# Kernel optimization log

Measured on AMD Instinct MI355X. Metric: run time of the kernel, lower is better.

## Reference

```python
import jax, jax.numpy as jnp
import numpy as np

N_HEAD = 16


def setup_inputs() -> dict:
    key = jax.random.key(0)
    k1, k2, k3 = jax.random.split(key, 3)
    B, S, D = 4, 2048, 1024
    scale = 1.0 / np.sqrt(D)
    return {
        "inp": jax.random.normal(k1, (B, S, D), dtype=jnp.float32),
        "w_attn": jax.random.normal(k2, (D, 3 * D), dtype=jnp.float32) * scale,
        "b_attn": jnp.zeros((3 * D,), dtype=jnp.float32),
        "w_proj": jax.random.normal(k3, (D, D), dtype=jnp.float32) * scale,
        "b_proj": jnp.zeros((D,), dtype=jnp.float32),
    }


def reference(inp, w_attn, b_attn, w_proj, b_proj):
    B, S, D = inp.shape
    H = N_HEAD
    hd = D // H
    qkv = inp @ w_attn + b_attn                      # [B,S,3D]
    q, k, v = jnp.split(qkv, 3, axis=-1)
    q = q.reshape(B, S, H, hd)
    k = k.reshape(B, S, H, hd)
    v = v.reshape(B, S, H, hd)
    # scores [B,H,S,S], scaled by 1/sqrt(head_dim)
    scores = jnp.einsum("bqhd,bkhd->bhqk", q, k) / jnp.sqrt(jnp.asarray(hd, dtype=inp.dtype))
    # causal mask: position q attends to k <= q
    causal = jnp.tril(jnp.ones((S, S), dtype=bool))
    scores = jnp.where(causal[None, None], scores, jnp.asarray(-jnp.inf, dtype=scores.dtype))
    probs = jax.nn.softmax(scores, axis=-1)          # dropout omitted (eval mode)
    ctx = jnp.einsum("bhqk,bkhd->bqhd", probs, v).reshape(B, S, D)
    return ctx @ w_proj + b_proj
```

## Files before the change

### kernel.cpp

```cpp
#include <hip/hip_runtime.h>


#define DEV __device__ __forceinline__

typedef unsigned short u16;
typedef unsigned u32x4 __attribute__((ext_vector_type(4)));
typedef u16   u16x8 __attribute__((ext_vector_type(8)));
typedef u16   u16x4 __attribute__((ext_vector_type(4)));
typedef float f32x4v __attribute__((ext_vector_type(4)));
typedef __bf16 bf16x8 __attribute__((ext_vector_type(8)));

#define BB 4
#define SS 2048
#define DD 1024
#define HH 16
#define HD 64
#define MM (BB*SS)
#define N3D (3*DD)
#define C8  0.18033688011112042f

DEV u16 f2bf(float f) { return __builtin_bit_cast(u16, (__bf16)f); }
DEV float bf2f(u16 h) { return __builtin_bit_cast(float, (unsigned)h << 16); }

DEV f32x4v mfma16(u16x8 a, u16x8 b, f32x4v c) {
  return __builtin_amdgcn_mfma_f32_16x16x32_bf16(
      __builtin_bit_cast(bf16x8, a), __builtin_bit_cast(bf16x8, b), c, 0, 0, 0);
}

DEV void async16(const void* g, void* l) {
  __builtin_amdgcn_global_load_lds(
      (const __attribute__((address_space(1))) void*)g,
      (__attribute__((address_space(3))) void*)l, 16, 0, 0);
}

#define WAIT_VM(N) asm volatile("s_waitcnt vmcnt(" #N ")" ::: "memory")
#define BAR() __builtin_amdgcn_s_barrier()

__global__ __launch_bounds__(256) void prep_kernel(
    const float* __restrict__ inp, const float* __restrict__ w_attn,
    const float* __restrict__ w_proj, u16* __restrict__ Abf,
    u16* __restrict__ WAt, u16* __restrict__ WPt) {
  const int bid = blockIdx.x;
  const int tid = threadIdx.x;
  if (bid < 4096) {
    __shared__ float t[32][33];
    const float* W; u16* Wt; int N, K, n0, k0;
    if (bid < 3072) { W = w_attn; Wt = WAt; N = N3D; K = DD;
                      n0 = (bid % 96) * 32; k0 = (bid / 96) * 32; }
    else            { W = w_proj; Wt = WPt; N = DD;  K = DD;
                      int tb = bid - 3072; n0 = (tb % 32) * 32; k0 = (tb / 32) * 32; }
    int tx = tid & 31, ty = tid >> 5;
    for (int i = ty; i < 32; i += 8)
      t[i][tx] = W[(long long)(k0 + i) * N + n0 + tx];
    __syncthreads();
    for (int i = ty; i < 32; i += 8)
      Wt[(long long)(n0 + i) * K + k0 + tx] = f2bf(t[tx][i]);
  } else {
    const long long n = (long long)MM * DD;
    long long i = (long long)(bid - 4096) * 256 + tid;
    for (long long j = i * 4; j < n; j += 2048LL * 256 * 4) {
      f32x4v v = *(const f32x4v*)(inp + j);
      u16x4 o;
      o.x = f2bf(v.x); o.y = f2bf(v.y); o.z = f2bf(v.z); o.w = f2bf(v.w);
      *(u16x4*)(Abf + j) = o;
    }
  }
}

__global__ __launch_bounds__(256) void gemm_kernel(
    const u16* __restrict__ A, const u16* __restrict__ Bt,
    const float* __restrict__ bias, void* __restrict__ Cout,
    u16* __restrict__ Vt, int Ndim, int Kdim, int mode) {
  __shared__ __align__(16) char smem[65536];

  const int tid = threadIdx.x;
  const int lane = tid & 63, wid = tid >> 6;
  const int l15 = lane & 15, lg = lane >> 4;

  const int orig = (int)(blockIdx.y * gridDim.x + blockIdx.x);
  const int xcd = orig & 7;
  const int c = orig >> 3;
  const int st = c >> 6;
  const int byl = (c & 63) >> 3;
  const int bxl = c & 7;
  const int bx = st * 8 + bxl;
  const int by = xcd * 8 + byl;
  const int rb = by * 128, cb = bx * 128;
  const int wr = (wid >> 1) * 64, wc = (wid & 1) * 64;

  f32x4v acc[4][4] = {};

  const int rlo = tid >> 3;
  const int cbS = (tid & 7) * 16;
  const int swS = cbS ^ ((rlo & 7) << 4);
  const int sd  = rlo * 128 + cbS;

  const int xr  = (l15 & 7) << 4;
  const int vaA = l15 * 128 + ((lg * 16) ^ xr);
  const int gvA0 = wr * 128 + vaA, gvA1 = gvA0 ^ 64;
  const int gvB0 = wc * 128 + vaA, gvB1 = gvB0 ^ 64;

  const char* pa[4];
  const char* pb[4];
#pragma unroll
  for (int i = 0; i < 4; ++i) {
    pa[i] = (const char*)A  + (long long)(rb + i * 32 + rlo) * (Kdim * 2) + swS;
    pb[i] = (const char*)Bt + (long long)(cb + i * 32 + rlo) * (Kdim * 2) + swS;
  }

  auto stage = [&](int dofs, int kb) {
#pragma unroll
    for (int i = 0; i < 4; ++i) {
      async16(pa[i] + kb, smem + dofs + i * 4096 + sd);
      async16(pb[i] + kb, smem + 32768 + dofs + i * 4096 + sd);
    }
  };

  auto compute = [&](int aofs, int bofs) {
    u16x8 a0[4], b0[4], a1[4], b1[4];
#pragma unroll
    for (int mi = 0; mi < 4; ++mi) {
      a0[mi] = *(const u16x8*)(smem + aofs + mi * 2048 + gvA0);
      a1[mi] = *(const u16x8*)(smem + aofs + mi * 2048 + gvA1);
    }
#pragma unroll
    for (int ni = 0; ni < 4; ++ni) {
      b0[ni] = *(const u16x8*)(smem + bofs + ni * 2048 + gvB0);
      b1[ni] = *(const u16x8*)(smem + bofs + ni * 2048 + gvB1);
    }
#pragma unroll
    for (int mi = 0; mi < 4; ++mi)
#pragma unroll
      for (int ni = 0; ni < 4; ++ni) {
        acc[mi][ni] = mfma16(a0[mi], b0[ni], acc[mi][ni]);
        acc[mi][ni] = mfma16(a1[mi], b1[ni], acc[mi][ni]);
      }
  };

  const int nK = Kdim >> 6;
  stage(0, 0);
  stage(16384, 128);
  int kt = 0;
  for (; kt + 2 < nK; kt += 2) {
    WAIT_VM(8); BAR();
    compute(0, 32768);
    BAR();
    stage(0, 256);
    WAIT_VM(8); BAR();
    compute(16384, 49152);
    BAR();
    stage(16384, 384);
#pragma unroll
    for (int i = 0; i < 4; ++i) { pa[i] += 256; pb[i] += 256; }
  }
  WAIT_VM(8); BAR();
  compute(0, 32768);
  WAIT_VM(0); BAR();
  compute(16384, 49152);

#pragma unroll
  for (int mi = 0; mi < 4; ++mi)
#pragma unroll
    for (int ni = 0; ni < 4; ++ni) {
      int col = cb + wc + ni * 16 + l15;
      float bv = bias[col];
      if (mode == 1 && col >= 2 * DD) {
        int h = (col >> 6) & 15, d = col & 63;
#pragma unroll
        for (int r = 0; r < 4; ++r) {
          int row = rb + wr + mi * 16 + lg * 4 + r;
          int b = row >> 11, s = row & 2047;
          Vt[(((long long)(b * HH + h) * HD + d) << 11) + s] = f2bf(acc[mi][ni][r] + bv);
        }
      } else {
        float sc = (mode == 1 && col < DD) ? C8 : 1.f;
#pragma unroll
        for (int r = 0; r < 4; ++r) {
          int row = rb + wr + mi * 16 + lg * 4 + r;
          float v = (acc[mi][ni][r] + bv) * sc;
          if (mode) ((u16*)Cout)[(long long)row * Ndim + col] = f2bf(v);
          else      ((float*)Cout)[(long long)row * Ndim + col] = v;
        }
      }
    }
}

__global__ __launch_bounds__(256, 4) void attn_kernel(
    const u16* __restrict__ qkv, const u16* __restrict__ Vt,
    u16* __restrict__ ctx) {
  __shared__ __align__(16) char smem[32768];

  const int tid = threadIdx.x, lane = tid & 63, wid = tid >> 6;
  const int l15 = lane & 15, lg = lane >> 4;

  const int d = (int)blockIdx.x;
  const int rank = d >> 3;
  const int t = rank >> 3;
  const int jj = t & 3, q4 = t >> 2;
  const int qt = (q4 == 0) ? 15 - jj : (q4 == 1) ? 8 + jj
               : (q4 == 2) ? 7 - jj  : jj;
  const int bh = (d & 7) * 8 + (rank & 7);
  const int b = bh >> 4, h = bh & 15;

  const u16* Qcol = qkv + (long long)b * SS * N3D + h * HD;
  const u16* Kcol = qkv + (long long)b * SS * N3D + DD + h * HD;
  const u16* Vbh  = Vt + (long long)bh * HD * SS;

  const u16x8 ones = {0x3F80, 0x3F80, 0x3F80, 0x3F80,
                      0x3F80, 0x3F80, 0x3F80, 0x3F80};

  const int rowA = 8 * (l15 >> 2) + (l15 & 3);
  const int kA = (((l15 & 3) | (((l15 >> 2) & 1) << 2))) << 4;
  const int vk0 = rowA * 128 + ((lg * 16) ^ kA);
  const int vk1 = vk0 ^ 64;
  const int vk2 = vk0 + 512;
  const int vk3 = vk2 ^ 64;
  const int kV = (((l15 & 3) | (((l15 >> 3) & 1) << 2))) << 4;
  const int vv0 = l15 * 128 + ((lg * 16) ^ kV);
  const int vv1 = vv0 ^ 64;

  const int rlo = tid >> 3;
  const int cbS = (tid & 7) * 16;
  const int kw = (((rlo & 3) | (((rlo >> 3) & 1) << 2))) << 4;
  const int swS = cbS ^ kw;
  const int sd  = rlo * 128 + cbS;
  const long long KSTP = 64LL * N3D * 2;
  const long long VSTP = 64LL * 2;
  const long long KHLF = 32LL * N3D * 2;
  const long long VHLF = 32LL * SS * 2;

  auto stage = [&](int dofs, const char* ka, const char* va) {
    async16(ka,        smem + dofs + sd);
    async16(ka + KHLF, smem + dofs + 4096 + sd);
    async16(va,        smem + 16384 + dofs + sd);
    async16(va + VHLF, smem + 16384 + dofs + 4096 + sd);
  };

  const int q0 = qt * 128;
  const int qw = q0 + wid * 32;
  const int nkb = 2 * qt + 2;

  u16x8 qf[2][2];
#pragma unroll
  for (int mi = 0; mi < 2; ++mi)
#pragma unroll
    for (int kk = 0; kk < 2; ++kk)
      qf[mi][kk] = *(const u16x8*)(Qcol + (long long)(qw + mi * 16 + l15) * N3D +
                                   kk * 32 + lg * 8);

  f32x4v acc[2][4] = {};
  f32x4v accl[2] = {};

  const char* ka = (const char*)Kcol + (long long)rlo * (N3D * 2) + swS;
  const char* va = (const char*)Vbh + (long long)rlo * (SS * 2) + swS;

  auto compute = [&](int kofs, int vofs, int kbase) {
    if (kbase > qw + 31) return;

    f32x4v pf[2][2][2] = {};
    {
      u16x8 kf0, kf1;
      kf0 = *(const u16x8*)(smem + kofs + vk0);
      kf1 = *(const u16x8*)(smem + kofs + vk1);
      __builtin_amdgcn_s_setprio(1);
      pf[0][0][0] = mfma16(kf0, qf[0][0], pf[0][0][0]);
      pf[0][0][0] = mfma16(kf1, qf[0][1], pf[0][0][0]);
      pf[1][0][0] = mfma16(kf0, qf[1][0], pf[1][0][0]);
      pf[1][0][0] = mfma16(kf1, qf[1][1], pf[1][0][0]);
      __builtin_amdgcn_s_setprio(0);
      kf0 = *(const u16x8*)(smem + kofs + vk2);
      kf1 = *(const u16x8*)(smem + kofs + vk3);
      __builtin_amdgcn_s_setprio(1);
      pf[0][0][1] = mfma16(kf0, qf[0][0], pf[0][0][1]);
      pf[0][0][1] = mfma16(kf1, qf[0][1], pf[0][0][1]);
      pf[1][0][1] = mfma16(kf0, qf[1][0], pf[1][0][1]);
      pf[1][0][1] = mfma16(kf1, qf[1][1], pf[1][0][1]);
      __builtin_amdgcn_s_setprio(0);
      kf0 = *(const u16x8*)(smem + kofs + 4096 + vk0);
      kf1 = *(const u16x8*)(smem + kofs + 4096 + vk1);
      __builtin_amdgcn_s_setprio(1);
      pf[0][1][0] = mfma16(kf0, qf[0][0], pf[0][1][0]);
      pf[0][1][0] = mfma16(kf1, qf[0][1], pf[0][1][0]);
      pf[1][1][0] = mfma16(kf0, qf[1][0], pf[1][1][0]);
      pf[1][1][0] = mfma16(kf1, qf[1][1], pf[1][1][0]);
      __builtin_amdgcn_s_setprio(0);
      kf0 = *(const u16x8*)(smem + kofs + 4096 + vk2);
      kf1 = *(const u16x8*)(smem + kofs + 4096 + vk3);
      __builtin_amdgcn_s_setprio(1);
      pf[0][1][1] = mfma16(kf0, qf[0][0], pf[0][1][1]);
      pf[0][1][1] = mfma16(kf1, qf[0][1], pf[0][1][1]);
      pf[1][1][1] = mfma16(kf0, qf[1][0], pf[1][1][1]);
      pf[1][1][1] = mfma16(kf1, qf[1][1], pf[1][1][1]);
      __builtin_amdgcn_s_setprio(0);
    }

    if (kbase + 63 > qw) {
      const int kl = kbase + lg * 8;
#pragma unroll
      for (int mi = 0; mi < 2; ++mi) {
        const int qg = qw + mi * 16 + l15;
#pragma unroll
        for (int ks = 0; ks < 2; ++ks)
#pragma unroll
          for (int ab = 0; ab < 2; ++ab)
#pragma unroll
            for (int r = 0; r < 4; ++r)
              if (kl + ks * 32 + ab * 4 + r > qg) pf[mi][ks][ab][r] = -1e30f;
      }
    }

#pragma unroll
    for (int mi = 0; mi < 2; ++mi)
#pragma unroll
      for (int ks = 0; ks < 2; ++ks)
#pragma unroll
        for (int ab = 0; ab < 2; ++ab)
#pragma unroll
          for (int r = 0; r < 4; ++r)
            pf[mi][ks][ab][r] = __builtin_exp2f(pf[mi][ks][ab][r]);

    u16x8 pa[2][2];
#pragma unroll
    for (int mi = 0; mi < 2; ++mi)
#pragma unroll
      for (int ks = 0; ks < 2; ++ks) {
        u32x4 w;
        w.x = (unsigned)f2bf(pf[mi][ks][0][0]) | ((unsigned)f2bf(pf[mi][ks][0][1]) << 16);
        w.y = (unsigned)f2bf(pf[mi][ks][0][2]) | ((unsigned)f2bf(pf[mi][ks][0][3]) << 16);
        w.z = (unsigned)f2bf(pf[mi][ks][1][0]) | ((unsigned)f2bf(pf[mi][ks][1][1]) << 16);
        w.w = (unsigned)f2bf(pf[mi][ks][1][2]) | ((unsigned)f2bf(pf[mi][ks][1][3]) << 16);
        pa[mi][ks] = __builtin_bit_cast(u16x8, w);
      }

    __builtin_amdgcn_s_setprio(1);
    accl[0] = mfma16(pa[0][0], ones, accl[0]);
    accl[0] = mfma16(pa[0][1], ones, accl[0]);
    accl[1] = mfma16(pa[1][0], ones, accl[1]);
    accl[1] = mfma16(pa[1][1], ones, accl[1]);
    __builtin_amdgcn_s_setprio(0);

#pragma unroll
    for (int di = 0; di < 4; ++di) {
      u16x8 v0 = *(const u16x8*)(smem + vofs + di * 2048 + vv0);
      u16x8 v1 = *(const u16x8*)(smem + vofs + di * 2048 + vv1);
      __builtin_amdgcn_s_setprio(1);
      acc[0][di] = mfma16(pa[0][0], v0, acc[0][di]);
      acc[0][di] = mfma16(pa[0][1], v1, acc[0][di]);
      acc[1][di] = mfma16(pa[1][0], v0, acc[1][di]);
      acc[1][di] = mfma16(pa[1][1], v1, acc[1][di]);
      __builtin_amdgcn_s_setprio(0);
    }
  };

  stage(0, ka, va);
  stage(8192, ka + KSTP, va + VSTP);

  int kb = 0;
  for (; kb + 2 < nkb; kb += 2) {
    WAIT_VM(4); BAR();
    compute(0, 16384, kb * 64);
    BAR();
    stage(0, ka + 2 * KSTP, va + 2 * VSTP);
    WAIT_VM(4); BAR();
    compute(8192, 24576, (kb + 1) * 64);
    BAR();
    stage(8192, ka + 3 * KSTP, va + 3 * VSTP);
    ka += 2 * KSTP; va += 2 * VSTP;
  }
  WAIT_VM(4); BAR();
  compute(0, 16384, kb * 64);
  WAIT_VM(0); BAR();
  compute(8192, 24576, (kb + 1) * 64);

#pragma unroll
  for (int mi = 0; mi < 2; ++mi)
#pragma unroll
    for (int r = 0; r < 4; ++r) {
      float inv = 1.f / accl[mi][r];
      int qrow = qw + mi * 16 + lg * 4 + r;
#pragma unroll
      for (int di = 0; di < 4; ++di) {
        int dd = di * 16 + l15;
        ctx[((long long)(b * SS + qrow)) * DD + h * HD + dd] = f2bf(acc[mi][di][r] * inv);
      }
    }
}

extern "C" void kernel_launch(void* const* d_in, const int* in_sizes, int n_in,
                              void* d_out, int out_size, void* d_ws, size_t ws_size,
                              hipStream_t stream) {
  const float* inp    = (const float*)d_in[0];
  const float* w_attn = (const float*)d_in[1];
  const float* b_attn = (const float*)d_in[2];
  const float* w_proj = (const float*)d_in[3];
  const float* b_proj = (const float*)d_in[4];
  float* out = (float*)d_out;
  char* ws = (char*)d_ws;

  const long long off_A   = 0;
  const long long off_WAt = 16777216;
  const long long off_WPt = 23068672;
  const long long off_qkv = 25165824;
  const long long off_ctx = 75497472;
  const long long off_Vt  = 92274688;
  const long long need    = 109051904;
  if (ws_size < (size_t)need) return;

  u16* Abf = (u16*)(ws + off_A);
  u16* WAt = (u16*)(ws + off_WAt);
  u16* WPt = (u16*)(ws + off_WPt);
  u16* qkv = (u16*)(ws + off_qkv);
  u16* ctx = (u16*)(ws + off_ctx);
  u16* Vt  = (u16*)(ws + off_Vt);

  prep_kernel<<<6144, 256, 0, stream>>>(inp, w_attn, w_proj, Abf, WAt, WPt);
  gemm_kernel<<<dim3(N3D / 128, MM / 128), 256, 0, stream>>>(
      Abf, WAt, b_attn, qkv, Vt, N3D, DD, 1);
  attn_kernel<<<1024, 256, 0, stream>>>(qkv, Vt, ctx);
  gemm_kernel<<<dim3(DD / 128, MM / 128), 256, 0, stream>>>(
      ctx, WPt, b_proj, out, nullptr, DD, DD, 0);
}
```

Before: 155.8 us.

## Split long causal attention tiles along KV and merge partials in a combine kernel

Query tiles 8–15 are now split into two work items along the key range. Each item writes unnormalized partial outputs in bf16 plus row sums to workspace, and a new combine kernel adds them and normalizes. A lookup table orders the work items longest-first to balance the load across 1536 blocks. This removes the tail imbalance of the causal workload, at the cost of an extra launch, extra global traffic, and bf16 rounding of the partials. Merging by plain sum of unnormalized outputs assumes the softmax uses a fixed scale with no running max.

```diff
diff --git a/kernel.cpp b/kernel.cpp
--- a/kernel.cpp
+++ b/kernel.cpp
@@ -35,6 +35,16 @@
 
 #define WAIT_VM(N) asm volatile("s_waitcnt vmcnt(" #N ")" ::: "memory")
 #define BAR() __builtin_amdgcn_s_barrier()
+
+#define IT(qt,k0,n,dst) ((qt)|((k0)<<4)|((n)<<9)|((dst)<<14))
+__device__ __constant__ int ITEM_TAB[24] = {
+  IT(15, 0,16,1), IT(15,16,16,2), IT(14, 0,16,1), IT( 7, 0,16,0),
+  IT(14,16,14,2), IT(13, 0,14,1), IT(13,14,14,2), IT(12, 0,14,1),
+  IT( 6, 0,14,0), IT(12,14,12,2), IT(11, 0,12,1), IT(11,12,12,2),
+  IT(10, 0,12,1), IT( 5, 0,12,0), IT(10,12,10,2), IT( 9, 0,10,1),
+  IT( 9,10,10,2), IT( 8, 0,10,1), IT( 4, 0,10,0), IT( 8,10, 8,2),
+  IT( 3, 0, 8,0), IT( 2, 0, 6,0), IT( 1, 0, 4,0), IT( 0, 0, 2,0)
+};
 
 __global__ __launch_bounds__(256) void prep_kernel(
     const float* __restrict__ inp, const float* __restrict__ w_attn,
@@ -187,7 +197,7 @@
 
 __global__ __launch_bounds__(256, 4) void attn_kernel(
     const u16* __restrict__ qkv, const u16* __restrict__ Vt,
-    u16* __restrict__ ctx) {
+    u16* __restrict__ ctx, u16* __restrict__ Ob, float* __restrict__ Lb) {
   __shared__ __align__(16) char smem[32768];
 
   const int tid = threadIdx.x, lane = tid & 63, wid = tid >> 6;
@@ -195,11 +205,13 @@
 
   const int d = (int)blockIdx.x;
   const int rank = d >> 3;
-  const int t = rank >> 3;
-  const int jj = t & 3, q4 = t >> 2;
-  const int qt = (q4 == 0) ? 15 - jj : (q4 == 1) ? 8 + jj
-               : (q4 == 2) ? 7 - jj  : jj;
+  const int item = rank >> 3;
   const int bh = (d & 7) * 8 + (rank & 7);
+  const int v = ITEM_TAB[item];
+  const int qt  = v & 15;
+  const int k0  = (v >> 4) & 31;
+  const int nkb = (v >> 9) & 31;
+  const int dst = (v >> 14) & 3;
   const int b = bh >> 4, h = bh & 15;
 
   const u16* Qcol = qkv + (long long)b * SS * N3D + h * HD;
@@ -238,7 +250,6 @@
 
   const int q0 = qt * 128;
   const int qw = q0 + wid * 32;
-  const int nkb = 2 * qt + 2;
 
   u16x8 qf[2][2];
 #pragma unroll
@@ -251,8 +262,8 @@
   f32x4v acc[2][4] = {};
   f32x4v accl[2] = {};
 
-  const char* ka = (const char*)Kcol + (long long)rlo * (N3D * 2) + swS;
-  const char* va = (const char*)Vbh + (long long)rlo * (SS * 2) + swS;
+  const char* ka = (const char*)Kcol + (long long)rlo * (N3D * 2) + swS + k0 * KSTP;
+  const char* va = (const char*)Vbh + (long long)rlo * (SS * 2) + swS + k0 * VSTP;
 
   auto compute = [&](int kofs, int vofs, int kbase) {
     if (kbase > qw + 31) return;
@@ -358,32 +369,71 @@
   int kb = 0;
   for (; kb + 2 < nkb; kb += 2) {
     WAIT_VM(4); BAR();
-    compute(0, 16384, kb * 64);
+    compute(0, 16384, (k0 + kb) * 64);
     BAR();
     stage(0, ka + 2 * KSTP, va + 2 * VSTP);
     WAIT_VM(4); BAR();
-    compute(8192, 24576, (kb + 1) * 64);
+    compute(8192, 24576, (k0 + kb + 1) * 64);
     BAR();
     stage(8192, ka + 3 * KSTP, va + 3 * VSTP);
     ka += 2 * KSTP; va += 2 * VSTP;
   }
   WAIT_VM(4); BAR();
-  compute(0, 16384, kb * 64);
+  compute(0, 16384, (k0 + kb) * 64);
   WAIT_VM(0); BAR();
-  compute(8192, 24576, (kb + 1) * 64);
-
-#pragma unroll
-  for (int mi = 0; mi < 2; ++mi)
-#pragma unroll
-    for (int r = 0; r < 4; ++r) {
-      float inv = 1.f / accl[mi][r];
-      int qrow = qw + mi * 16 + lg * 4 + r;
-#pragma unroll
-      for (int di = 0; di < 4; ++di) {
-        int dd = di * 16 + l15;
-        ctx[((long long)(b * SS + qrow)) * DD + h * HD + dd] = f2bf(acc[mi][di][r] * inv);
-      }
-    }
+  compute(8192, 24576, (k0 + kb + 1) * 64);
+
+  if (dst == 0) {
+#pragma unroll
+    for (int mi = 0; mi < 2; ++mi)
+#pragma unroll
+      for (int r = 0; r < 4; ++r) {
+        float inv = 1.f / accl[mi][r];
+        int qrow = qw + mi * 16 + lg * 4 + r;
+#pragma unroll
+        for (int di = 0; di < 4; ++di) {
+          int dd = di * 16 + l15;
+          ctx[((long long)(b * SS + qrow)) * DD + h * HD + dd] = f2bf(acc[mi][di][r] * inv);
+        }
+      }
+  } else {
+    const int si = (bh * 8 + (qt - 8)) * 2 + (dst - 1);
+    u16* Obt = Ob + (long long)si * 8192;
+#pragma unroll
+    for (int mi = 0; mi < 2; ++mi)
+#pragma unroll
+      for (int r = 0; r < 4; ++r) {
+        int lrow = wid * 32 + mi * 16 + lg * 4 + r;
+#pragma unroll
+        for (int di = 0; di < 4; ++di)
+          Obt[lrow * 64 + di * 16 + l15] = f2bf(acc[mi][di][r]);
+        if (l15 == 0) Lb[si * 128 + lrow] = accl[mi][r];
+      }
+  }
+}
+
+__global__ __launch_bounds__(256) void combine_kernel(
+    const u16* __restrict__ Ob, const float* __restrict__ Lb,
+    u16* __restrict__ ctx) {
+  const int tile = (int)blockIdx.x;
+  const int bh = tile >> 3, qt = 8 + (tile & 7);
+  const int b = bh >> 4, h = bh & 15;
+  const long long o0 = (long long)(tile * 2) * 8192;
+  const long long o1 = o0 + 8192;
+  const int l0 = tile * 2 * 128, l1 = l0 + 128;
+#pragma unroll
+  for (int j = 0; j < 4; ++j) {
+    int e = ((int)threadIdx.x * 4 + j) * 8;
+    int lrow = e >> 6, d0 = e & 63;
+    u16x8 a = *(const u16x8*)(Ob + o0 + e);
+    u16x8 c = *(const u16x8*)(Ob + o1 + e);
+    float inv = 1.f / (Lb[l0 + lrow] + Lb[l1 + lrow]);
+    u16x8 o;
+#pragma unroll
+    for (int i = 0; i < 8; ++i)
+      o[i] = f2bf((bf2f(a[i]) + bf2f(c[i])) * inv);
+    *(u16x8*)(ctx + ((long long)(b * SS + qt * 128 + lrow)) * DD + h * HD + d0) = o;
+  }
 }
 
 extern "C" void kernel_launch(void* const* d_in, const int* in_sizes, int n_in,
@@ -412,11 +462,14 @@
   u16* qkv = (u16*)(ws + off_qkv);
   u16* ctx = (u16*)(ws + off_ctx);
   u16* Vt  = (u16*)(ws + off_Vt);
+  u16*   Ob = (u16*)(ws + 0);
+  float* Lb = (float*)(ws + 17825792);
 
   prep_kernel<<<6144, 256, 0, stream>>>(inp, w_attn, w_proj, Abf, WAt, WPt);
   gemm_kernel<<<dim3(N3D / 128, MM / 128), 256, 0, stream>>>(
       Abf, WAt, b_attn, qkv, Vt, N3D, DD, 1);
-  attn_kernel<<<1024, 256, 0, stream>>>(qkv, Vt, ctx);
+  attn_kernel<<<1536, 256, 0, stream>>>(qkv, Vt, ctx, Ob, Lb);
+  combine_kernel<<<512, 256, 0, stream>>>(Ob, Lb, ctx);
   gemm_kernel<<<dim3(DD / 128, MM / 128), 256, 0, stream>>>(
       ctx, WPt, b_proj, out, nullptr, DD, DD, 0);
 }
```

Result: slower. 162.4 us (+4.2%).
